# Performance work log

Measured on AMD Instinct MI355X. Metric: run time of the kernel, lower is better.

Reference implementation:

```python
import jax, jax.numpy as jnp
import numpy as np

B, N, D, H = 8, 1024, 768, 12
DH = D // H
DFF = 4 * D
EPS = 1e-5


def setup_inputs() -> dict:
    key = jax.random.key(0)
    ks = jax.random.split(key, 16)
    s = 0.02
    return {
        "x": jax.random.normal(ks[0], (B, N, D), jnp.float32),
        "ln1_g": jnp.ones((D,), jnp.float32),
        "ln1_b": jnp.zeros((D,), jnp.float32),
        "wqkv": jax.random.normal(ks[1], (D, 3 * D), jnp.float32) * s,
        "bqkv": jnp.zeros((3 * D,), jnp.float32),
        "wo": jax.random.normal(ks[2], (D, D), jnp.float32) * s,
        "bo": jnp.zeros((D,), jnp.float32),
        "rel_bias": jax.random.normal(ks[3], (H, N, N), jnp.float32) * s,
        "ln2_g": jnp.ones((D,), jnp.float32),
        "ln2_b": jnp.zeros((D,), jnp.float32),
        "w1": jax.random.normal(ks[4], (D, DFF), jnp.float32) * s,
        "b1": jnp.zeros((DFF,), jnp.float32),
        "w2": jax.random.normal(ks[5], (DFF, D), jnp.float32) * s,
        "b2": jnp.zeros((D,), jnp.float32),
    }


def _layer_norm(x, g, b):
    mu = jnp.mean(x, axis=-1, keepdims=True)
    var = jnp.mean(jnp.square(x - mu), axis=-1, keepdims=True)
    return (x - mu) * jax.lax.rsqrt(var + EPS) * g + b


def reference(x, ln1_g, ln1_b, wqkv, bqkv, wo, bo, rel_bias, ln2_g, ln2_b, w1, b1, w2, b2):
    # --- pre-norm self-attention with relative position bias + residual ---
    h = _layer_norm(x, ln1_g, ln1_b)
    qkv = h @ wqkv + bqkv                      # [B, N, 3D]
    qkv = qkv.reshape(B, N, 3, H, DH)
    q, k, v = qkv[:, :, 0], qkv[:, :, 1], qkv[:, :, 2]  # each [B, N, H, DH]
    scale = 1.0 / jnp.sqrt(jnp.asarray(DH, x.dtype))
    scores = jnp.einsum("bnhd,bmhd->bhnm", q, k) * scale + rel_bias[None]
    attn = jax.nn.softmax(scores, axis=-1)
    ctx = jnp.einsum("bhnm,bmhd->bnhd", attn, v).reshape(B, N, D)
    x = ctx @ wo + bo + x
    # --- pre-norm FFN (GELU) + residual ---
    h = _layer_norm(x, ln2_g, ln2_b)
    h = jax.nn.gelu(h @ w1 + b1)
    x = h @ w2 + b2 + x
    return x
```

## Files before the change

kernel.cpp:

```cpp
#include <hip/hip_runtime.h>
#include <hip/hip_bf16.h>
#include <math.h>

#define D_MODEL 768
#define NTOK    8192
#define SEQ     1024
#define NH      12
#define DHD     64
#define DFF     3072

typedef __attribute__((ext_vector_type(8)))  __bf16 bf16x8;
typedef __attribute__((ext_vector_type(4)))  float  f32x4;
typedef __attribute__((ext_vector_type(16))) float  f32x16;
typedef __attribute__((ext_vector_type(4)))  unsigned short us4;

typedef const __attribute__((address_space(1))) void g_void;
typedef __attribute__((address_space(3))) void lds_void;

__device__ __forceinline__ unsigned short f2bf(float f) {
  unsigned u = __float_as_uint(f);
  u += 0x7fffu + ((u >> 16) & 1u);
  return (unsigned short)(u >> 16);
}

__device__ __forceinline__ f32x4 mfma16(bf16x8 a, bf16x8 b, f32x4 c) {
  return __builtin_amdgcn_mfma_f32_16x16x32_bf16(a, b, c, 0, 0, 0);
}
__device__ __forceinline__ f32x16 mfma32(bf16x8 a, bf16x8 b, f32x16 c) {
  return __builtin_amdgcn_mfma_f32_32x32x16_bf16(a, b, c, 0, 0, 0);
}

__device__ __forceinline__ void gload_lds16(const unsigned short* g, unsigned short* l) {
  __builtin_amdgcn_global_load_lds((g_void*)g, (lds_void*)l, 16, 0, 0);
}

__device__ __forceinline__ void plswap(unsigned &a, unsigned &b) {
  asm("v_permlane32_swap_b32 %0, %1" : "+v"(a), "+v"(b));
}
__device__ __forceinline__ bf16x8 mk8(unsigned a, unsigned b, unsigned c, unsigned d) {
  union { unsigned u[4]; bf16x8 v; } t;
  t.u[0] = a; t.u[1] = b; t.u[2] = c; t.u[3] = d;
  return t.v;
}

__global__ __launch_bounds__(256)
void ln_kernel(const float* __restrict__ x, const float* __restrict__ gam,
               const float* __restrict__ bet, unsigned short* __restrict__ out) {
  const int w = threadIdx.x >> 6, lane = threadIdx.x & 63;
  const size_t row = (size_t)blockIdx.x * 4 + w;
  const float* xr = x + row * D_MODEL;
  f32x4 v[3];
#pragma unroll
  for (int c = 0; c < 3; ++c) v[c] = *(const f32x4*)(xr + c * 256 + lane * 4);
  float s = 0.f;
#pragma unroll
  for (int c = 0; c < 3; ++c)
#pragma unroll
    for (int j = 0; j < 4; ++j) s += v[c][j];
#pragma unroll
  for (int o = 32; o; o >>= 1) s += __shfl_xor(s, o);
  const float mu = s * (1.0f / D_MODEL);
  float vs = 0.f;
#pragma unroll
  for (int c = 0; c < 3; ++c)
#pragma unroll
    for (int j = 0; j < 4; ++j) { float d = v[c][j] - mu; vs += d * d; }
#pragma unroll
  for (int o = 32; o; o >>= 1) vs += __shfl_xor(vs, o);
  const float rs = rsqrtf(vs * (1.0f / D_MODEL) + 1e-5f);
  unsigned short* orow = out + row * D_MODEL;
#pragma unroll
  for (int c = 0; c < 3; ++c) {
    us4 o4;
#pragma unroll
    for (int j = 0; j < 4; ++j) {
      int idx = c * 256 + lane * 4 + j;
      o4[j] = f2bf((v[c][j] - mu) * rs * gam[idx] + bet[idx]);
    }
    *(us4*)(orow + c * 256 + lane * 4) = o4;
  }
}

__global__ __launch_bounds__(256)
void wtrans_kernel(const float* __restrict__ W, unsigned short* __restrict__ Wt,
                   int K, int Nc) {
  __shared__ float t[32][33];
  const int tx = threadIdx.x & 31, ty = threadIdx.x >> 5;
  const int nb = blockIdx.x * 32, kb = blockIdx.y * 32;
#pragma unroll
  for (int i = 0; i < 4; ++i)
    t[ty + 8 * i][tx] = W[(size_t)(kb + ty + 8 * i) * Nc + nb + tx];
  __syncthreads();
#pragma unroll
  for (int i = 0; i < 4; ++i)
    Wt[(size_t)(nb + ty + 8 * i) * K + kb + tx] = f2bf(t[tx][ty + 8 * i]);
}

__global__ __launch_bounds__(256)
void brelayout_kernel(const float* __restrict__ rel, unsigned short* __restrict__ bF) {
  const int gw = blockIdx.x * 4 + (threadIdx.x >> 6);
  const int lane = threadIdx.x & 63;
  const int ktg = gw & 31, qt = (gw >> 5) & 31, h = gw >> 10;
  const int q = qt * 32 + (lane & 31), hi = lane >> 5;
  const float* src = rel + ((size_t)h * SEQ + q) * SEQ + ktg * 32 + 4 * hi;
  const float L2E = 1.4426950408889634f;
  unsigned ow[8];
#pragma unroll
  for (int g = 0; g < 4; ++g) {
    f32x4 v = *(const f32x4*)(src + g * 8);
    asm("v_cvt_pk_bf16_f32 %0, %1, %2" : "=v"(ow[2 * g])     : "v"(v[0] * L2E), "v"(v[1] * L2E));
    asm("v_cvt_pk_bf16_f32 %0, %1, %2" : "=v"(ow[2 * g + 1]) : "v"(v[2] * L2E), "v"(v[3] * L2E));
  }
  unsigned short* dst = bF + (((size_t)gw) * 64 + lane) * 16;
  *(uint4*)(dst)     = make_uint4(ow[0], ow[1], ow[2], ow[3]);
  *(uint4*)(dst + 8) = make_uint4(ow[4], ow[5], ow[6], ow[7]);
}

#define MODE_QKV  0
#define MODE_PROJ 1
#define MODE_FFN1 2
#define MODE_FFN2 3

template <int MODE>
__global__ __launch_bounds__(256)
void gemm_bt(const unsigned short* __restrict__ A, const unsigned short* __restrict__ Bt,
             int K, const float* __restrict__ bias, const float* __restrict__ resid,
             float* __restrict__ outF, unsigned short* __restrict__ o0,
             unsigned short* __restrict__ o1, unsigned short* __restrict__ o2) {
  __shared__ alignas(16) unsigned short smem[2][2][128 * 64];
  const int tid = threadIdx.x;
  const int w = tid >> 6, lane = tid & 63;
  const int l31 = lane & 31, hi = lane >> 5;
  const int wm = w >> 1, wn = w & 1;
  const int nwg = gridDim.x * gridDim.y;
  const int bid0 = blockIdx.y * gridDim.x + blockIdx.x;
  const int cpx = nwg >> 3;
  const int bid = (bid0 & 7) * cpx + (bid0 >> 3);
  const int bx = bid % gridDim.x, by = bid / gridDim.x;
  const size_t m0 = (size_t)by * 128;
  const size_t n0 = (size_t)bx * 128;
  const unsigned short* gA = A + m0 * K;
  const unsigned short* gB = Bt + n0 * K;

  const int r8 = lane >> 3;
  const int u8 = lane & 7;
  const int ucol = (u8 ^ r8) * 8;

  f32x16 acc[2][2];
#pragma unroll
  for (int i = 0; i < 2; ++i)
#pragma unroll
    for (int j = 0; j < 2; ++j) acc[i][j] = (f32x16)(0.f);
  const int nk = K >> 6;

  auto stage = [&](int buf, int kt) {
#pragma unroll
    for (int g = 0; g < 4; ++g) {
      const int rowb = w * 32 + g * 8;
      gload_lds16(gA + (size_t)(rowb + r8) * K + kt * 64 + ucol, &smem[0][buf][rowb * 64]);
      gload_lds16(gB + (size_t)(rowb + r8) * K + kt * 64 + ucol, &smem[1][buf][rowb * 64]);
    }
  };

  const int swr = l31 & 7;
  const int rA = (wm * 64 + l31) * 64;
  const int rB = (wn * 64 + l31) * 64;

  stage(0, 0);
  __syncthreads();
  for (int kt = 0; kt < nk; ++kt) {
    const int buf = kt & 1;
    if (kt + 1 < nk) stage(buf ^ 1, kt + 1);
    bf16x8 af[2][4], bf[2][4];
#pragma unroll
    for (int mt = 0; mt < 2; ++mt)
#pragma unroll
      for (int ks = 0; ks < 4; ++ks) {
        af[mt][ks] = *(const bf16x8*)&smem[0][buf][rA + mt * 2048 + (((ks * 2 + hi) ^ swr) * 8)];
        bf[mt][ks] = *(const bf16x8*)&smem[1][buf][rB + mt * 2048 + (((ks * 2 + hi) ^ swr) * 8)];
      }
#pragma unroll
    for (int mt = 0; mt < 2; ++mt)
#pragma unroll
      for (int nt = 0; nt < 2; ++nt)
#pragma unroll
        for (int ks = 0; ks < 4; ++ks)
          acc[mt][nt] = mfma32(af[mt][ks], bf[nt][ks], acc[mt][nt]);
    __syncthreads();
  }

  if constexpr (MODE == MODE_QKV) {
    if (bx >= 12) {
      unsigned short* tb = &smem[0][0][0];
#pragma unroll
      for (int mt = 0; mt < 2; ++mt)
#pragma unroll
        for (int nt = 0; nt < 2; ++nt)
#pragma unroll
          for (int r = 0; r < 16; ++r) {
            const int nl = wn * 64 + nt * 32 + l31;
            const int ml = wm * 64 + mt * 32 + (r & 3) + 8 * (r >> 2) + 4 * hi;
            tb[nl * 136 + ml] = f2bf(acc[mt][nt][r] + bias[(int)n0 + nl]);
          }
      __syncthreads();
      const int rr = tid & 127, half = tid >> 7;
      const int n2 = ((int)n0 - 1536) + rr;
      const int hh = n2 >> 6, dh = n2 & 63;
      const int b2 = (int)(m0 >> 10), nq0 = (int)(m0 & 1023);
      unsigned short* dst = o2 + ((size_t)(b2 * NH + hh) * DHD + dh) * SEQ + nq0 + half * 64;
      const unsigned short* src = tb + rr * 136 + half * 64;
#pragma unroll
      for (int i = 0; i < 4; ++i)
        *(uint4*)(dst + i * 8) = *(const uint4*)(src + i * 8);
      return;
    }
  }

#pragma unroll
  for (int mt = 0; mt < 2; ++mt) {
#pragma unroll
    for (int nt = 0; nt < 2; ++nt) {
#pragma unroll
      for (int r = 0; r < 16; ++r) {
        const int m = (int)m0 + wm * 64 + mt * 32 + (r & 3) + 8 * (r >> 2) + 4 * hi;
        const int n = (int)n0 + wn * 64 + nt * 32 + l31;
        float v = acc[mt][nt][r] + bias[n];
        if constexpr (MODE == MODE_QKV) {
          const int b = m >> 10, nq = m & 1023;
          if (n < 768) {
            const int h = n >> 6, dh = n & 63;
            o0[(((size_t)(b * NH + h)) * SEQ + nq) * DHD + dh] =
                f2bf(v * 0.1803368801111244f);
          } else {
            const int n2 = n - 768, h = n2 >> 6, dh = n2 & 63;
            o1[(((size_t)(b * NH + h)) * SEQ + nq) * DHD + dh] = f2bf(v);
          }
        } else if constexpr (MODE == MODE_PROJ) {
          const size_t off = (size_t)m * D_MODEL + n;
          outF[off] = v + resid[off];
        } else if constexpr (MODE == MODE_FFN1) {
          const float e = __expf(-1.5957691216057308f * (v + 0.044715f * v * v * v));
          o0[(size_t)m * DFF + n] = f2bf(v / (1.0f + e));
        } else {
          const size_t off = (size_t)m * D_MODEL + n;
          outF[off] = v + resid[off];
        }
      }
    }
  }
}

__global__ __launch_bounds__(256, 4)
void attn_kernel(const unsigned short* __restrict__ q, const unsigned short* __restrict__ k,
                 const unsigned short* __restrict__ vt, const unsigned short* __restrict__ bF,
                 unsigned short* __restrict__ ctx) {
  __shared__ alignas(16) unsigned short kv[2][16][64 * 8];
  const int tid = threadIdx.x, w = tid >> 6, lane = tid & 63;
  const int l31 = lane & 31, hi = lane >> 5;
  const int bid = (blockIdx.x & 7) * 96 + (blockIdx.x >> 3);
  const int bh = bid >> 3, qblk = bid & 7;
  const int b = bh / NH, h = bh % NH;
  const int q0w = qblk * 128 + w * 32;
  const unsigned short* qp = q + (size_t)bh * SEQ * DHD;
  const unsigned short* kp = k + (size_t)bh * SEQ * DHD;
  const unsigned short* vp = vt + (size_t)bh * DHD * SEQ;
  const unsigned short* bfp = bF + ((((size_t)(h * 32 + qblk * 4 + w)) * 32) * 64 + lane) * 16;

  bf16x8 Qf[4];
#pragma unroll
  for (int ds = 0; ds < 4; ++ds)
    Qf[ds] = *(const bf16x8*)(qp + (size_t)(q0w + l31) * DHD + ds * 16 + hi * 8);

  f32x16 o[2];
#pragma unroll
  for (int dt = 0; dt < 2; ++dt) o[dt] = (f32x16)(0.f);
  float mrun = -INFINITY, lrun = 0.f;

  auto stage = [&](int buf, int kb) {
    if (w < 2) {
      const unsigned short* g0 = kp + (size_t)(kb * 64 + w * 32 + l31) * DHD + hi * 8;
#pragma unroll
      for (int ds = 0; ds < 4; ++ds)
        gload_lds16(g0 + ds * 16, &kv[buf][w * 4 + ds][0]);
    } else {
      const int dt = w - 2;
      const unsigned short* g0 = vp + (size_t)(dt * 32 + l31) * SEQ + kb * 64 + hi * 8;
#pragma unroll
      for (int kh = 0; kh < 4; ++kh)
        gload_lds16(g0 + kh * 16, &kv[buf][8 + dt * 4 + kh][0]);
    }
  };

  stage(0, 0);
  __syncthreads();
  for (int kb = 0; kb < SEQ / 64; ++kb) {
    const int buf = kb & 1;
    if (kb + 1 < SEQ / 64) stage(buf ^ 1, kb + 1);

    f32x16 s0 = (f32x16)(0.f), s1 = (f32x16)(0.f);
    __builtin_amdgcn_s_setprio(1);
#pragma unroll
    for (int ds = 0; ds < 4; ++ds) {
      bf16x8 kf0 = *(const bf16x8*)&kv[buf][ds][lane * 8];
      s0 = mfma32(kf0, Qf[ds], s0);
      bf16x8 kf1 = *(const bf16x8*)&kv[buf][4 + ds][lane * 8];
      s1 = mfma32(kf1, Qf[ds], s1);
    }
    __builtin_amdgcn_s_setprio(0);

    const unsigned short* bb = bfp + (size_t)(kb * 2) * 64 * 16;
    uint4 a0 = *(const uint4*)(bb),            a1 = *(const uint4*)(bb + 8);
    uint4 c0 = *(const uint4*)(bb + 64 * 16),  c1 = *(const uint4*)(bb + 64 * 16 + 8);
    unsigned uw0[8] = {a0.x, a0.y, a0.z, a0.w, a1.x, a1.y, a1.z, a1.w};
    unsigned uw1[8] = {c0.x, c0.y, c0.z, c0.w, c1.x, c1.y, c1.z, c1.w};
    float p0[16], p1[16];
#pragma unroll
    for (int j = 0; j < 8; ++j) {
      p0[2 * j]     = s0[2 * j]     + __uint_as_float(uw0[j] << 16);
      p0[2 * j + 1] = s0[2 * j + 1] + __uint_as_float(uw0[j] & 0xffff0000u);
      p1[2 * j]     = s1[2 * j]     + __uint_as_float(uw1[j] << 16);
      p1[2 * j + 1] = s1[2 * j + 1] + __uint_as_float(uw1[j] & 0xffff0000u);
    }

    float pmax = p0[0];
#pragma unroll
    for (int i = 1; i < 16; ++i) pmax = fmaxf(pmax, p0[i]);
#pragma unroll
    for (int i = 0; i < 16; ++i) pmax = fmaxf(pmax, p1[i]);
    if (!__all(pmax - mrun <= 11.0f)) {
      float pm = fmaxf(pmax, __shfl_xor(pmax, 32));
      const float mn = fmaxf(mrun, pm);
      const float al = __builtin_amdgcn_exp2f(mrun - mn);
      mrun = mn;
      lrun *= al;
#pragma unroll
      for (int dt = 0; dt < 2; ++dt)
#pragma unroll
        for (int r = 0; r < 16; ++r) o[dt][r] *= al;
    }
#pragma unroll
    for (int i = 0; i < 16; ++i) { p0[i] = __builtin_amdgcn_exp2f(p0[i] - mrun); lrun += p0[i]; }
#pragma unroll
    for (int i = 0; i < 16; ++i) { p1[i] = __builtin_amdgcn_exp2f(p1[i] - mrun); lrun += p1[i]; }

    unsigned wpk[16];
#pragma unroll
    for (int i = 0; i < 8; ++i) {
      asm("v_cvt_pk_bf16_f32 %0, %1, %2" : "=v"(wpk[i])     : "v"(p0[2 * i]), "v"(p0[2 * i + 1]));
      asm("v_cvt_pk_bf16_f32 %0, %1, %2" : "=v"(wpk[8 + i]) : "v"(p1[2 * i]), "v"(p1[2 * i + 1]));
    }
    plswap(wpk[0], wpk[2]);   plswap(wpk[1], wpk[3]);
    plswap(wpk[4], wpk[6]);   plswap(wpk[5], wpk[7]);
    plswap(wpk[8], wpk[10]);  plswap(wpk[9], wpk[11]);
    plswap(wpk[12], wpk[14]); plswap(wpk[13], wpk[15]);
    bf16x8 pf[4];
    pf[0] = mk8(wpk[0], wpk[1], wpk[2], wpk[3]);
    pf[1] = mk8(wpk[4], wpk[5], wpk[6], wpk[7]);
    pf[2] = mk8(wpk[8], wpk[9], wpk[10], wpk[11]);
    pf[3] = mk8(wpk[12], wpk[13], wpk[14], wpk[15]);

    __builtin_amdgcn_s_setprio(1);
#pragma unroll
    for (int dt = 0; dt < 2; ++dt)
#pragma unroll
      for (int kh = 0; kh < 4; ++kh) {
        bf16x8 vf = *(const bf16x8*)&kv[buf][8 + dt * 4 + kh][lane * 8];
        o[dt] = mfma32(vf, pf[kh], o[dt]);
      }
    __builtin_amdgcn_s_setprio(0);

    __syncthreads();
  }

  lrun += __shfl_xor(lrun, 32);
  const float inv = 1.0f / lrun;
  unsigned short* crow = ctx + ((size_t)b * SEQ + q0w + l31) * D_MODEL + h * DHD;
#pragma unroll
  for (int dt = 0; dt < 2; ++dt)
#pragma unroll
    for (int g = 0; g < 4; ++g) {
      us4 ov;
#pragma unroll
      for (int j = 0; j < 4; ++j) ov[j] = f2bf(o[dt][4 * g + j] * inv);
      *(us4*)(crow + dt * 32 + g * 8 + 4 * hi) = ov;
    }
}

extern "C" void kernel_launch(void* const* d_in, const int* in_sizes, int n_in,
                              void* d_out, int out_size, void* d_ws, size_t ws_size,
                              hipStream_t stream) {
  (void)in_sizes; (void)n_in; (void)out_size; (void)ws_size;
  const float* x     = (const float*)d_in[0];
  const float* ln1_g = (const float*)d_in[1];
  const float* ln1_b = (const float*)d_in[2];
  const float* wqkv  = (const float*)d_in[3];
  const float* bqkv  = (const float*)d_in[4];
  const float* wo    = (const float*)d_in[5];
  const float* bo    = (const float*)d_in[6];
  const float* rel   = (const float*)d_in[7];
  const float* ln2_g = (const float*)d_in[8];
  const float* ln2_b = (const float*)d_in[9];
  const float* w1    = (const float*)d_in[10];
  const float* b1    = (const float*)d_in[11];
  const float* w2    = (const float*)d_in[12];
  const float* b2    = (const float*)d_in[13];
  float* out = (float*)d_out;

  char* p = (char*)d_ws;
  auto take = [&](size_t bytes) {
    void* r = (void*)p;
    p += (bytes + 255) & ~(size_t)255;
    return r;
  };
  unsigned short* hbuf  = (unsigned short*)take((size_t)NTOK * D_MODEL * 2);
  unsigned short* wqkvT = (unsigned short*)take((size_t)2304 * 768 * 2);
  unsigned short* woT   = (unsigned short*)take((size_t)768 * 768 * 2);
  unsigned short* w1T   = (unsigned short*)take((size_t)3072 * 768 * 2);
  unsigned short* w2T   = (unsigned short*)take((size_t)768 * 3072 * 2);
  unsigned short* qbuf  = (unsigned short*)take((size_t)8 * NH * SEQ * DHD * 2);
  unsigned short* kbuf  = (unsigned short*)take((size_t)8 * NH * SEQ * DHD * 2);
  unsigned short* vtbuf = (unsigned short*)take((size_t)8 * NH * SEQ * DHD * 2);
  unsigned short* ctxb  = (unsigned short*)take((size_t)NTOK * D_MODEL * 2);
  unsigned short* h1buf = (unsigned short*)take((size_t)NTOK * DFF * 2);
  unsigned short* biasF = h1buf;

  wtrans_kernel<<<dim3(2304 / 32, 768 / 32), 256, 0, stream>>>(wqkv, wqkvT, 768, 2304);
  wtrans_kernel<<<dim3(768 / 32, 768 / 32), 256, 0, stream>>>(wo, woT, 768, 768);
  wtrans_kernel<<<dim3(3072 / 32, 768 / 32), 256, 0, stream>>>(w1, w1T, 768, 3072);
  wtrans_kernel<<<dim3(768 / 32, 3072 / 32), 256, 0, stream>>>(w2, w2T, 3072, 768);
  brelayout_kernel<<<NH * 32 * 32 / 4, 256, 0, stream>>>(rel, biasF);

  ln_kernel<<<NTOK / 4, 256, 0, stream>>>(x, ln1_g, ln1_b, hbuf);
  gemm_bt<MODE_QKV><<<dim3(2304 / 128, NTOK / 128), 256, 0, stream>>>(
      hbuf, wqkvT, 768, bqkv, nullptr, nullptr, qbuf, kbuf, vtbuf);
  attn_kernel<<<8 * NH * (SEQ / 128), 256, 0, stream>>>(qbuf, kbuf, vtbuf, biasF, ctxb);
  gemm_bt<MODE_PROJ><<<dim3(768 / 128, NTOK / 128), 256, 0, stream>>>(
      ctxb, woT, 768, bo, x, out, nullptr, nullptr, nullptr);
  ln_kernel<<<NTOK / 4, 256, 0, stream>>>(out, ln2_g, ln2_b, hbuf);
  gemm_bt<MODE_FFN1><<<dim3(DFF / 128, NTOK / 128), 256, 0, stream>>>(
      hbuf, w1T, 768, b1, nullptr, nullptr, h1buf, nullptr, nullptr);
  gemm_bt<MODE_FFN2><<<dim3(768 / 128, NTOK / 128), 256, 0, stream>>>(
      h1buf, w2T, 3072, b2, out, out, nullptr, nullptr, nullptr);
}
```

Measured before the change: 274.8 us.

## Triple-buffer GEMM K-loop with BK=32, vmcnt waits, and MFMA priority

Restructures the bf16 GEMM main loop from a double-buffered K tile of 64 to a triple-buffered K tile of 32, prefetching two stages ahead. Plain __syncthreads is replaced with explicit vmcnt waits plus s_barrier, and s_setprio is raised around the MFMA block. The smaller LDS footprint allows a launch bound of 3 blocks per CU. The aim is to hide global-load latency and raise occupancy, at the cost of more loop iterations and barriers per K. The swizzle is adjusted to the narrower row.

Result: slower. 298.9 us (+8.8%).

```diff
diff --git a/kernel.cpp b/kernel.cpp
--- a/kernel.cpp
+++ b/kernel.cpp
@@ -122,12 +122,12 @@
 #define MODE_FFN2 3
 
 template <int MODE>
-__global__ __launch_bounds__(256)
+__global__ __launch_bounds__(256, 3)
 void gemm_bt(const unsigned short* __restrict__ A, const unsigned short* __restrict__ Bt,
              int K, const float* __restrict__ bias, const float* __restrict__ resid,
              float* __restrict__ outF, unsigned short* __restrict__ o0,
              unsigned short* __restrict__ o1, unsigned short* __restrict__ o2) {
-  __shared__ alignas(16) unsigned short smem[2][2][128 * 64];
+  __shared__ alignas(16) unsigned short smem[2][3][128 * 32];
   const int tid = threadIdx.x;
   const int w = tid >> 6, lane = tid & 63;
   const int l31 = lane & 31, hi = lane >> 5;
@@ -142,51 +142,60 @@
   const unsigned short* gA = A + m0 * K;
   const unsigned short* gB = Bt + n0 * K;
 
-  const int r8 = lane >> 3;
-  const int u8 = lane & 7;
-  const int ucol = (u8 ^ r8) * 8;
+  const int r16 = lane >> 2;
+  const int u4 = lane & 3;
+  const int ucol = (u4 ^ (r16 & 3)) * 8;
 
   f32x16 acc[2][2];
 #pragma unroll
   for (int i = 0; i < 2; ++i)
 #pragma unroll
     for (int j = 0; j < 2; ++j) acc[i][j] = (f32x16)(0.f);
-  const int nk = K >> 6;
+  const int nk = K >> 5;
 
   auto stage = [&](int buf, int kt) {
 #pragma unroll
-    for (int g = 0; g < 4; ++g) {
-      const int rowb = w * 32 + g * 8;
-      gload_lds16(gA + (size_t)(rowb + r8) * K + kt * 64 + ucol, &smem[0][buf][rowb * 64]);
-      gload_lds16(gB + (size_t)(rowb + r8) * K + kt * 64 + ucol, &smem[1][buf][rowb * 64]);
+    for (int g = 0; g < 2; ++g) {
+      const int rowb = w * 32 + g * 16;
+      gload_lds16(gA + (size_t)(rowb + r16) * K + kt * 32 + ucol, &smem[0][buf][rowb * 32]);
+      gload_lds16(gB + (size_t)(rowb + r16) * K + kt * 32 + ucol, &smem[1][buf][rowb * 32]);
     }
   };
 
-  const int swr = l31 & 7;
-  const int rA = (wm * 64 + l31) * 64;
-  const int rB = (wn * 64 + l31) * 64;
+  const int swr = l31 & 3;
+  const int rA = (wm * 64 + l31) * 32;
+  const int rB = (wn * 64 + l31) * 32;
 
   stage(0, 0);
-  __syncthreads();
+  stage(1, 1);
+  asm volatile("s_waitcnt vmcnt(4)" ::: "memory");
+  __builtin_amdgcn_s_barrier();
+
+  int bcur = 0;
   for (int kt = 0; kt < nk; ++kt) {
-    const int buf = kt & 1;
-    if (kt + 1 < nk) stage(buf ^ 1, kt + 1);
-    bf16x8 af[2][4], bf[2][4];
+    const int bpre = (bcur == 0) ? 2 : bcur - 1;
+    if (kt + 2 < nk) stage(bpre, kt + 2);
+    bf16x8 af[2][2], bf[2][2];
 #pragma unroll
     for (int mt = 0; mt < 2; ++mt)
 #pragma unroll
-      for (int ks = 0; ks < 4; ++ks) {
-        af[mt][ks] = *(const bf16x8*)&smem[0][buf][rA + mt * 2048 + (((ks * 2 + hi) ^ swr) * 8)];
-        bf[mt][ks] = *(const bf16x8*)&smem[1][buf][rB + mt * 2048 + (((ks * 2 + hi) ^ swr) * 8)];
+      for (int ks = 0; ks < 2; ++ks) {
+        af[mt][ks] = *(const bf16x8*)&smem[0][bcur][rA + mt * 1024 + (((ks * 2 + hi) ^ swr) * 8)];
+        bf[mt][ks] = *(const bf16x8*)&smem[1][bcur][rB + mt * 1024 + (((ks * 2 + hi) ^ swr) * 8)];
       }
+    __builtin_amdgcn_s_setprio(1);
 #pragma unroll
     for (int mt = 0; mt < 2; ++mt)
 #pragma unroll
       for (int nt = 0; nt < 2; ++nt)
 #pragma unroll
-        for (int ks = 0; ks < 4; ++ks)
+        for (int ks = 0; ks < 2; ++ks)
           acc[mt][nt] = mfma32(af[mt][ks], bf[nt][ks], acc[mt][nt]);
-    __syncthreads();
+    __builtin_amdgcn_s_setprio(0);
+    if (kt + 2 < nk) asm volatile("s_waitcnt vmcnt(4)" ::: "memory");
+    else             asm volatile("s_waitcnt vmcnt(0)" ::: "memory");
+    __builtin_amdgcn_s_barrier();
+    bcur = (bcur == 2) ? 0 : bcur + 1;
   }
 
   if constexpr (MODE == MODE_QKV) {
```

## Use 512-thread 8-wave GEMM kernel for projection and FFN layers

Applied to the files above, without the earlier changes.

Adds a new GEMM kernel with 512 threads (8 waves in a 2x4 grid, each computing a 64x32 sub-tile) and a double-buffered 128x128x64 LDS tile loaded directly from global memory. It also swizzles block IDs across 8 groups and raises wave priority around the MFMA section. The projection, FFN1 and FFN2 GEMMs now use it, while QKV stays on the old kernel. The GELU epilogue is rewritten with exp2 and a hardware reciprocal, which trades a little accuracy for fewer instructions. Each wave holds fewer accumulators, so more waves can overlap memory with compute, but each wave reuses less data from LDS.

Measured after the change: 281.5 us. 1.02x slower.

```diff
diff --git a/kernel.cpp b/kernel.cpp
--- a/kernel.cpp
+++ b/kernel.cpp
@@ -23,9 +23,6 @@
   return (unsigned short)(u >> 16);
 }
 
-__device__ __forceinline__ f32x4 mfma16(bf16x8 a, bf16x8 b, f32x4 c) {
-  return __builtin_amdgcn_mfma_f32_16x16x32_bf16(a, b, c, 0, 0, 0);
-}
 __device__ __forceinline__ f32x16 mfma32(bf16x8 a, bf16x8 b, f32x16 c) {
   return __builtin_amdgcn_mfma_f32_32x32x16_bf16(a, b, c, 0, 0, 0);
 }
@@ -238,13 +235,92 @@
         } else if constexpr (MODE == MODE_PROJ) {
           const size_t off = (size_t)m * D_MODEL + n;
           outF[off] = v + resid[off];
-        } else if constexpr (MODE == MODE_FFN1) {
-          const float e = __expf(-1.5957691216057308f * (v + 0.044715f * v * v * v));
-          o0[(size_t)m * DFF + n] = f2bf(v / (1.0f + e));
-        } else {
-          const size_t off = (size_t)m * D_MODEL + n;
-          outF[off] = v + resid[off];
         }
+      }
+    }
+  }
+}
+
+template <int MODE>
+__global__ __launch_bounds__(512)
+void gemm512(const unsigned short* __restrict__ A, const unsigned short* __restrict__ Bt,
+             int K, const float* __restrict__ bias, const float* __restrict__ resid,
+             float* __restrict__ outF, unsigned short* __restrict__ o0) {
+  __shared__ alignas(16) unsigned short smem[2][2][128 * 64];
+  const int tid = threadIdx.x;
+  const int w = tid >> 6, lane = tid & 63;
+  const int l31 = lane & 31, hi = lane >> 5;
+  const int wm = w >> 2, wn = w & 3;
+  const int nwg = gridDim.x * gridDim.y;
+  const int bid0 = blockIdx.y * gridDim.x + blockIdx.x;
+  const int cpx = nwg >> 3;
+  const int bid = (bid0 & 7) * cpx + (bid0 >> 3);
+  const int bx = bid % gridDim.x, by = bid / gridDim.x;
+  const size_t m0 = (size_t)by * 128;
+  const size_t n0 = (size_t)bx * 128;
+  const unsigned short* gA = A + m0 * K;
+  const unsigned short* gB = Bt + n0 * K;
+
+  const int r8 = lane >> 3;
+  const int u8 = lane & 7;
+  const int ucol = (u8 ^ r8) * 8;
+
+  f32x16 acc[2];
+  acc[0] = (f32x16)(0.f);
+  acc[1] = (f32x16)(0.f);
+  const int nk = K >> 6;
+
+  auto stage = [&](int buf, int kt) {
+#pragma unroll
+    for (int g = 0; g < 2; ++g) {
+      const int rowb = w * 16 + g * 8;
+      gload_lds16(gA + (size_t)(rowb + r8) * K + kt * 64 + ucol, &smem[0][buf][rowb * 64]);
+      gload_lds16(gB + (size_t)(rowb + r8) * K + kt * 64 + ucol, &smem[1][buf][rowb * 64]);
+    }
+  };
+
+  const int swr = l31 & 7;
+  const int rA = (wm * 64 + l31) * 64;
+  const int rB = (wn * 32 + l31) * 64;
+
+  stage(0, 0);
+  __syncthreads();
+  for (int kt = 0; kt < nk; ++kt) {
+    const int buf = kt & 1;
+    if (kt + 1 < nk) stage(buf ^ 1, kt + 1);
+    bf16x8 af[2][4], bf[4];
+#pragma unroll
+    for (int ks = 0; ks < 4; ++ks) {
+      const int uo = ((ks * 2 + hi) ^ swr) * 8;
+      af[0][ks] = *(const bf16x8*)&smem[0][buf][rA + uo];
+      af[1][ks] = *(const bf16x8*)&smem[0][buf][rA + 2048 + uo];
+      bf[ks]    = *(const bf16x8*)&smem[1][buf][rB + uo];
+    }
+    __builtin_amdgcn_s_setprio(1);
+#pragma unroll
+    for (int mt = 0; mt < 2; ++mt)
+#pragma unroll
+      for (int ks = 0; ks < 4; ++ks)
+        acc[mt] = mfma32(af[mt][ks], bf[ks], acc[mt]);
+    __builtin_amdgcn_s_setprio(0);
+    __syncthreads();
+  }
+
+#pragma unroll
+  for (int mt = 0; mt < 2; ++mt) {
+#pragma unroll
+    for (int r = 0; r < 16; ++r) {
+      const int m = (int)m0 + wm * 64 + mt * 32 + (r & 3) + 8 * (r >> 2) + 4 * hi;
+      const int n = (int)n0 + wn * 32 + l31;
+      float v = acc[mt][r] + bias[n];
+      if constexpr (MODE == MODE_FFN1) {
+        const float t = v * v;
+        const float s = fmaf(-0.10295276f, t, -2.3022164f);
+        const float e = __builtin_amdgcn_exp2f(v * s);
+        o0[(size_t)m * DFF + n] = f2bf(v * __builtin_amdgcn_rcpf(1.0f + e));
+      } else {
+        const size_t off = (size_t)m * D_MODEL + n;
+        outF[off] = v + resid[off];
       }
     }
   }
@@ -434,11 +510,11 @@
   gemm_bt<MODE_QKV><<<dim3(2304 / 128, NTOK / 128), 256, 0, stream>>>(
       hbuf, wqkvT, 768, bqkv, nullptr, nullptr, qbuf, kbuf, vtbuf);
   attn_kernel<<<8 * NH * (SEQ / 128), 256, 0, stream>>>(qbuf, kbuf, vtbuf, biasF, ctxb);
-  gemm_bt<MODE_PROJ><<<dim3(768 / 128, NTOK / 128), 256, 0, stream>>>(
-      ctxb, woT, 768, bo, x, out, nullptr, nullptr, nullptr);
+  gemm512<MODE_PROJ><<<dim3(768 / 128, NTOK / 128), 512, 0, stream>>>(
+      ctxb, woT, 768, bo, x, out, nullptr);
   ln_kernel<<<NTOK / 4, 256, 0, stream>>>(out, ln2_g, ln2_b, hbuf);
-  gemm_bt<MODE_FFN1><<<dim3(DFF / 128, NTOK / 128), 256, 0, stream>>>(
-      hbuf, w1T, 768, b1, nullptr, nullptr, h1buf, nullptr, nullptr);
-  gemm_bt<MODE_FFN2><<<dim3(768 / 128, NTOK / 128), 256, 0, stream>>>(
-      h1buf, w2T, 3072, b2, out, out, nullptr, nullptr, nullptr);
-}
+  gemm512<MODE_FFN1><<<dim3(DFF / 128, NTOK / 128), 512, 0, stream>>>(
+      hbuf, w1T, 768, b1, nullptr, nullptr, h1buf);
+  gemm512<MODE_FFN2><<<dim3(768 / 128, NTOK / 128), 512, 0, stream>>>(
+      h1buf, w2T, 3072, b2, out, out, nullptr);
+}
```
